# Kernel optimization log

Measured on AMD Instinct MI355X. Metric: run time of the kernel, lower is better.

Reference implementation:

```python
import jax, jax.numpy as jnp
import numpy as np

NUM_SAMPLES = 10
MIN_DIST_PTS = 8
TOP_K = 10
GRID_SIZE = 4
GAP = 0.1


def sample_line_points(seg):
    # seg: [N,2,2] (endpoints, ij coords). Vectorized version of the per-group linspace loop.
    lengths = jnp.linalg.norm(seg[:, 0] - seg[:, 1], axis=1)
    n_samp = jnp.clip(jnp.floor(lengths / MIN_DIST_PTS), 2, NUM_SAMPLES)  # [N]
    t = jnp.arange(NUM_SAMPLES, dtype=seg.dtype)  # [S]
    interval = (seg[:, 1] - seg[:, 0]) / (n_samp[:, None] - 1)  # [N,2]
    pts = seg[:, None, 0, :] + t[None, :, None] * interval[:, None, :]  # [N,S,2]
    valid = t[None, :] < n_samp[:, None]  # [N,S]
    pts = jnp.where(valid[..., None], pts, 0.0)  # original zero-pads invalid samples
    return pts, valid


def grid_sample_norm(desc, pts, img_size):
    # desc: [D,Hc,Wc]; pts: [P,2] (i,j) pixel coords in image of size img_size=(H,W).
    # Replicates kornia normalize_pixel_coordinates + F.grid_sample(align_corners=False,
    # bilinear, zero padding), then L2-normalize along D.
    D, Hc, Wc = desc.shape
    H, W = img_size
    gx = 2.0 * pts[:, 1] / (W - 1) - 1.0
    gy = 2.0 * pts[:, 0] / (H - 1) - 1.0
    ix = ((gx + 1.0) * Wc - 1.0) / 2.0
    iy = ((gy + 1.0) * Hc - 1.0) / 2.0
    x0 = jnp.floor(ix)
    y0 = jnp.floor(iy)
    wx1 = ix - x0
    wy1 = iy - y0
    x0i = x0.astype(jnp.int32)
    y0i = y0.astype(jnp.int32)

    def gather(yi, xi):
        inb = (xi >= 0) & (xi < Wc) & (yi >= 0) & (yi < Hc)
        v = desc[:, jnp.clip(yi, 0, Hc - 1), jnp.clip(xi, 0, Wc - 1)]  # [D,P]
        return v * inb

    v = (gather(y0i, x0i) * (1 - wy1) * (1 - wx1)
         + gather(y0i, x0i + 1) * (1 - wy1) * wx1
         + gather(y0i + 1, x0i) * wy1 * (1 - wx1)
         + gather(y0i + 1, x0i + 1) * wy1 * wx1)
    nrm = jnp.linalg.norm(v, axis=0, keepdims=True)
    return v / jnp.maximum(nrm, 1e-12)


def needleman_wunsch(scores):
    # scores: [B,n,m]. Row-wise scan; the within-row dependency
    # v[j+1]=max(v[j], max(prev[j+1], prev[j]+s)) is a prefix-max (cummax).
    b, n, m = scores.shape
    s = scores - GAP
    init = jnp.zeros((b, m + 1), s.dtype)

    def step(prev, row):  # prev [B,m+1], row [B,m]
        a = jnp.maximum(prev[:, 1:], prev[:, :-1] + row)
        new = jnp.maximum(jax.lax.cummax(a, axis=1), 0.0)
        return jnp.concatenate([jnp.zeros((b, 1), s.dtype), new], axis=1), None

    final, _ = jax.lax.scan(step, init, jnp.swapaxes(s, 0, 1))
    return final[:, -1]


def nw_candidate_scores(scores):
    # scores: [N1,N2,S,S] -> (nw [N1,2k], topk [N1,k])
    ls1 = jnp.max(scores, axis=3)
    v1 = ls1 != -1
    ls1 = jnp.where(v1, ls1, 0.0).sum(2) / v1.sum(2)
    ls2 = jnp.max(scores, axis=2)
    v2 = ls2 != -1
    ls2 = jnp.where(v2, ls2, 0.0).sum(2) / v2.sum(2)
    line_scores = (ls1 + ls2) / 2
    topk = jnp.argsort(line_scores, axis=1)[:, -TOP_K:]  # [N1,k]
    top_scores = jnp.take_along_axis(scores, topk[:, :, None, None], axis=1)  # [N1,k,S,S]
    top_scores = jnp.concatenate([top_scores, jnp.flip(top_scores, axis=-1)], axis=1)  # [N1,2k,S,S]
    N1, t2k, n, m = top_scores.shape
    nw = needleman_wunsch(top_scores.reshape(N1 * t2k, n, m)).reshape(N1, t2k)
    return nw, topk


def filter_and_match(scores):
    nw, topk = nw_candidate_scores(scores)
    t2k = nw.shape[1]
    best = jnp.argmax(nw, axis=1) % (t2k // 2)
    return jnp.take_along_axis(topk, best[:, None], axis=1)[:, 0]


def compute_scores(line_seg1, line_seg2, desc1, desc2):
    S = NUM_SAMPLES
    img1 = (desc1.shape[2] * GRID_SIZE, desc1.shape[3] * GRID_SIZE)
    img2 = (desc2.shape[2] * GRID_SIZE, desc2.shape[3] * GRID_SIZE)
    pts1, val1 = sample_line_points(line_seg1)
    pts2, val2 = sample_line_points(line_seg2)
    d1 = grid_sample_norm(desc1[0], pts1.reshape(-1, 2), img1)  # [D, N1*S]
    d2 = grid_sample_norm(desc2[0], pts2.reshape(-1, 2), img2)  # [D, N2*S]
    sc = d1.T @ d2  # [N1*S, N2*S]
    sc = jnp.where(val1.reshape(-1)[:, None], sc, -1.0)
    sc = jnp.where(val2.reshape(-1)[None, :], sc, -1.0)
    N1, N2 = line_seg1.shape[0], line_seg2.shape[0]
    return sc.reshape(N1, S, N2, S).transpose(0, 2, 1, 3)  # [N1,N2,S,S]


def reference(line_seg1, line_seg2, desc1, desc2):
    scores = compute_scores(line_seg1, line_seg2, desc1, desc2)
    matches = filter_and_match(scores)
    # cross check
    matches2 = filter_and_match(scores.transpose(1, 0, 3, 2))
    mutual = matches2[matches] == jnp.arange(line_seg1.shape[0])
    return jnp.where(mutual, matches, -1).astype(jnp.int32)


def setup_inputs() -> dict:
    key = jax.random.key(0)
    k1, k2, k3, k4 = jax.random.split(key, 4)
    IMG = 512.0
    line_seg1 = jax.random.uniform(k1, (512, 2, 2), dtype=jnp.float32) * (IMG - 1.0)
    line_seg2 = jax.random.uniform(k2, (512, 2, 2), dtype=jnp.float32) * (IMG - 1.0)
    desc1 = jax.random.normal(k3, (1, 128, 128, 128), dtype=jnp.float32)
    desc2 = jax.random.normal(k4, (1, 128, 128, 128), dtype=jnp.float32)
    return {"line_seg1": line_seg1, "line_seg2": line_seg2, "desc1": desc1, "desc2": desc2}
```

## Files before the change

### kernel.cpp

```cpp
#include <hip/hip_runtime.h>
#include <cmath>

#define NL 512
#define SS 10
#define DD 128
#define HWC (128 * 128)

typedef _Float16 f16x8 __attribute__((ext_vector_type(8)));
typedef float f32x4 __attribute__((ext_vector_type(4)));

__device__ __forceinline__ void gload_lds16(const void* g, void* l)
{
    __builtin_amdgcn_global_load_lds(
        (__attribute__((address_space(1))) void*)const_cast<void*>(g),
        (__attribute__((address_space(3))) void*)l, 16, 0, 0);
}

__global__ __launch_bounds__(256) void transpose_kernel(
    const float* __restrict__ in1, const float* __restrict__ in2,
    float* __restrict__ out1, float* __restrict__ out2)
{
    const float* in = blockIdx.z ? in2 : in1;
    float* out = blockIdx.z ? out2 : out1;
    __shared__ float tile[32][33];
    int hw0 = blockIdx.x * 32;
    int d0 = blockIdx.y * 32;
    int tx = threadIdx.x, ty = threadIdx.y;
#pragma unroll
    for (int j = 0; j < 32; j += 8)
        tile[ty + j][tx] = in[(size_t)(d0 + ty + j) * HWC + hw0 + tx];
    __syncthreads();
#pragma unroll
    for (int j = 0; j < 32; j += 8)
        out[(size_t)(hw0 + ty + j) * DD + d0 + tx] = tile[tx][ty + j];
}

__device__ __forceinline__ float fetchd(const float* __restrict__ dt, int y, int x, int d)
{
    bool inb = (x >= 0) && (x < 128) && (y >= 0) && (y < 128);
    int yc = y < 0 ? 0 : (y > 127 ? 127 : y);
    int xc = x < 0 ? 0 : (x > 127 ? 127 : x);
    float v = dt[((size_t)(yc * 128 + xc)) * DD + d];
    return inb ? v : 0.0f;
}

__global__ __launch_bounds__(256) void sample_kernel(
    const float* __restrict__ seg1, const float* __restrict__ seg2,
    const float* __restrict__ dt1, const float* __restrict__ dt2,
    float* __restrict__ dd1, float* __restrict__ dd2,
    _Float16* __restrict__ h1, _Float16* __restrict__ m1,
    _Float16* __restrict__ h2, _Float16* __restrict__ m2,
    int* __restrict__ v1, int* __restrict__ v2)
{
#pragma clang fp contract(off)
    int L = blockIdx.x;
    int img = blockIdx.y;
    const float* seg = img ? seg2 : seg1;
    const float* dt = img ? dt2 : dt1;
    float* dd = img ? dd2 : dd1;
    _Float16* ph = img ? h2 : h1;
    _Float16* pm = img ? m2 : m1;
    int* vv = img ? v2 : v1;

    float p0y = seg[L * 4 + 0], p0x = seg[L * 4 + 1];
    float p1y = seg[L * 4 + 2], p1x = seg[L * 4 + 3];
    float dy = p0y - p1y, dx = p0x - p1x;
    float len = sqrtf(dy * dy + dx * dx);
    float nf = floorf(len / 8.0f);
    nf = fminf(fmaxf(nf, 2.0f), 10.0f);
    int ni = (int)nf;
    float ivy = (p1y - p0y) / (nf - 1.0f);
    float ivx = (p1x - p0x) / (nf - 1.0f);

    int tid = threadIdx.x;
    int g = tid >> 7;
    int d = tid & 127;
    __shared__ float redw[4];

    for (int it = 0; it < 5; ++it) {
        int t = it * 2 + g;
        int pt = L * SS + t;
        bool val = t < ni;
        float v = 0.0f, s = 0.0f;
        if (val) {
            float py = p0y + (float)t * ivy;
            float px = p0x + (float)t * ivx;
            float gx = 2.0f * px / 511.0f - 1.0f;
            float gy = 2.0f * py / 511.0f - 1.0f;
            float ix = ((gx + 1.0f) * 128.0f - 1.0f) / 2.0f;
            float iy = ((gy + 1.0f) * 128.0f - 1.0f) / 2.0f;
            float x0f = floorf(ix), y0f = floorf(iy);
            float wx = ix - x0f, wy = iy - y0f;
            int x0 = (int)x0f, y0 = (int)y0f;
            float g00 = fetchd(dt, y0, x0, d);
            float g01 = fetchd(dt, y0, x0 + 1, d);
            float g10 = fetchd(dt, y0 + 1, x0, d);
            float g11 = fetchd(dt, y0 + 1, x0 + 1, d);
            float omwx = 1.0f - wx, omwy = 1.0f - wy;
            v = g00 * omwy * omwx + g01 * omwy * wx + g10 * wy * omwx + g11 * wy * wx;
            s = v * v;
        }
#pragma unroll
        for (int m = 1; m < 64; m <<= 1) s += __shfl_xor(s, m);
        if ((tid & 63) == 0) redw[tid >> 6] = s;
        __syncthreads();
        float outv = 0.0f;
        if (val) {
            float nrm = sqrtf(redw[2 * g] + redw[2 * g + 1]);
            outv = v / fmaxf(nrm, 1e-12f);
        }
        dd[(size_t)pt * DD + d] = outv;
        float xs = outv * 256.0f;
        _Float16 hh = (_Float16)xs;
        float r1 = xs - (float)hh;
        _Float16 mm = (_Float16)r1;
        int po = ((pt >> 4) << 11) + ((d >> 3) << 7) + ((pt & 15) << 3) + (d & 7);
        ph[po] = hh;
        pm[po] = mm;
        if (d == 0) vv[pt] = val ? 1 : 0;
        __syncthreads();
    }
}

__device__ __forceinline__ void stage_ks(
    const _Float16* __restrict__ ah, const _Float16* __restrict__ am,
    const _Float16* __restrict__ bh, const _Float16* __restrict__ bm,
    int bi, int bj, int ks, int wave, int lane, char* dst)
{
#pragma unroll
    for (int c = 0; c < 10; ++c) {
        int chunk = wave * 10 + c;
        int side = chunk >= 20;
        int rem = side ? chunk - 20 : chunk;
        int plane = rem >= 10;
        int pb = plane ? rem - 10 : rem;
        const _Float16* base = side ? (plane ? bm : bh) : (plane ? am : ah);
        size_t off = ((size_t)((side ? bj : bi) * 10 + pb) << 11) + (ks << 9) + (lane << 3);
        gload_lds16(base + off, dst + (chunk << 10));
    }
}

__global__ __launch_bounds__(256, 2) void gemm_ls_kernel(
    const _Float16* __restrict__ ah_, const _Float16* __restrict__ am_,
    const _Float16* __restrict__ bh_, const _Float16* __restrict__ bm_,
    const int* __restrict__ v1, const int* __restrict__ v2,
    float* __restrict__ ls, float* __restrict__ lsT)
{
    __shared__ __align__(16) char smem[81920];
    int tid = threadIdx.x;
    int wave = tid >> 6, lane = tid & 63;
    int wr = wave >> 1, wc = wave & 1;

    int flat = blockIdx.y * 32 + blockIdx.x;
    int xcd = flat & 7, n = flat >> 3;
    int bi = (xcd >> 1) * 8 + (n >> 4);
    int bj = (xcd & 1) * 16 + (n & 15);

    int fro = ((lane >> 4) << 8) + ((lane & 15) << 4);

    f32x4 zz = {0.0f, 0.0f, 0.0f, 0.0f};
    f32x4 acc[5][5];
#pragma unroll
    for (int i = 0; i < 5; ++i)
#pragma unroll
        for (int j = 0; j < 5; ++j) acc[i][j] = zz;

    stage_ks(ah_, am_, bh_, bm_, bi, bj, 0, wave, lane, smem);

#pragma unroll 1
    for (int ks = 0; ks < 4; ++ks) {
        char* buf = smem + ((ks & 1) ? 40960 : 0);
        if (ks < 3) {
            stage_ks(ah_, am_, bh_, bm_, bi, bj, ks + 1, wave, lane,
                     smem + (((ks + 1) & 1) ? 40960 : 0));
            asm volatile("s_waitcnt vmcnt(10)" ::: "memory");
        } else {
            asm volatile("s_waitcnt vmcnt(0)" ::: "memory");
        }
        __builtin_amdgcn_sched_barrier(0);
        __builtin_amdgcn_s_barrier();
        __builtin_amdgcn_sched_barrier(0);

        f16x8 B0[5], B1[5];
#pragma unroll
        for (int j = 0; j < 5; ++j) {
            int pb = wc * 5 + j;
            B0[j] = *(const f16x8*)(buf + ((20 + pb) << 10) + fro);
            B1[j] = *(const f16x8*)(buf + ((30 + pb) << 10) + fro);
        }
#pragma unroll
        for (int i = 0; i < 5; ++i) {
            int pb = wr * 5 + i;
            f16x8 fh = *(const f16x8*)(buf + (pb << 10) + fro);
            f16x8 fm = *(const f16x8*)(buf + ((10 + pb) << 10) + fro);
#pragma unroll
            for (int j = 0; j < 5; ++j) {
                f32x4 t = acc[i][j];
                t = __builtin_amdgcn_mfma_f32_16x16x32_f16(fh, B0[j], t, 0, 0, 0);
                t = __builtin_amdgcn_mfma_f32_16x16x32_f16(fh, B1[j], t, 0, 0, 0);
                t = __builtin_amdgcn_mfma_f32_16x16x32_f16(fm, B0[j], t, 0, 0, 0);
                acc[i][j] = t;
            }
        }
        __builtin_amdgcn_sched_barrier(0);
        __builtin_amdgcn_s_barrier();
        __builtin_amdgcn_sched_barrier(0);
    }

    float* scr = (float*)smem;
    const float rescale = 1.0f / 65536.0f;
    for (int half = 0; half < 2; ++half) {
        __syncthreads();
        if (wr == half) {
            float* reg = scr + wc * 6464;
#pragma unroll
            for (int i = 0; i < 5; ++i)
#pragma unroll
                for (int j = 0; j < 5; ++j)
#pragma unroll
                    for (int r = 0; r < 4; ++r) {
                        int row = i * 16 + ((lane >> 4) << 2) + r;
                        int col = j * 16 + (lane & 15);
                        int pi = row / 10, s = row - pi * 10;
                        int pj = col / 10, t = col - pj * 10;
                        reg[(pi * 8 + pj) * 101 + s * 10 + t] = acc[i][j][r] * rescale;
                    }
            asm volatile("s_waitcnt lgkmcnt(0)" ::: "memory");
            const float* mp = reg + lane * 101;
            int iL = bi * 16 + half * 8 + (lane >> 3);
            int jL = bj * 16 + wc * 8 + (lane & 7);
            int va[10], vb[10];
#pragma unroll
            for (int s = 0; s < 10; ++s) va[s] = v1[iL * 10 + s];
#pragma unroll
            for (int t = 0; t < 10; ++t) vb[t] = v2[jL * 10 + t];
            float cmx[10];
#pragma unroll
            for (int t = 0; t < 10; ++t) cmx[t] = -3.0e38f;
            float sum1 = 0.0f; int c1 = 0;
#pragma unroll
            for (int s = 0; s < 10; ++s) {
                float rmx = -3.0e38f;
#pragma unroll
                for (int t = 0; t < 10; ++t) {
                    float v = (va[s] && vb[t]) ? mp[s * 10 + t] : -1.0f;
                    rmx = fmaxf(rmx, v);
                    cmx[t] = fmaxf(cmx[t], v);
                }
                if (rmx != -1.0f) { sum1 += rmx; c1++; }
            }
            float sum2 = 0.0f; int c2 = 0;
#pragma unroll
            for (int t = 0; t < 10; ++t) {
                if (cmx[t] != -1.0f) { sum2 += cmx[t]; c2++; }
            }
            float out = (sum1 / (float)c1 + sum2 / (float)c2) * 0.5f;
            ls[(size_t)iL * NL + jL] = out;
            lsT[(size_t)jL * NL + iL] = out;
        }
    }
}

__global__ __launch_bounds__(64) void topk_kernel(
    const float* __restrict__ ls, const float* __restrict__ lsT, int* __restrict__ topk)
{
    int i = blockIdx.x;
    int dir = blockIdx.y;
    int lane = threadIdx.x;
    const float* src = dir ? &lsT[(size_t)i * NL] : &ls[(size_t)i * NL];

    float v[8];
#pragma unroll
    for (int it = 0; it < 8; ++it) v[it] = src[it * 64 + lane];
    int* outp = &topk[(size_t)(dir * NL + i) * 10];

    for (int p = 9; p >= 0; --p) {
        float bv = -3.0e38f;
        int bi = -1;
#pragma unroll
        for (int it = 0; it < 8; ++it) {
            int j = it * 64 + lane;
            bool better = (v[it] > bv) || (v[it] == bv && j > bi);
            if (better) { bv = v[it]; bi = j; }
        }
#pragma unroll
        for (int m = 1; m < 64; m <<= 1) {
            float ov = __shfl_xor(bv, m);
            int oi = __shfl_xor(bi, m);
            bool better = (ov > bv) || (ov == bv && oi > bi);
            if (better) { bv = ov; bi = oi; }
        }
        if ((bi & 63) == lane) v[bi >> 6] = -3.0e38f;
        if (lane == 0) outp[p] = bi;
    }
}

__global__ __launch_bounds__(128) void nw_kernel(
    const float* __restrict__ d1, const float* __restrict__ d2,
    const int* __restrict__ v1, const int* __restrict__ v2,
    const int* __restrict__ topk, float* __restrict__ nwout)
{
    int L = blockIdx.x;
    int dir = blockIdx.y;
    const float* Ad = dir ? d2 : d1;
    const float* Bd = dir ? d1 : d2;
    const int* vA = dir ? v2 : v1;
    const int* vB = dir ? v1 : v2;
    const int* tk = topk + (size_t)(dir * NL + L) * 10;

    __shared__ float Asl[10 * 132];
    __shared__ float Bsl[10 * 132];
    __shared__ float M[10][110];
    __shared__ int vam[10];

    int tid = threadIdx.x;
#pragma unroll
    for (int it = 0; it < 10; ++it) {
        int idx = tid + it * 128;
        int row = idx >> 7, col = idx & 127;
        Asl[row * 132 + col] = Ad[((size_t)L * 10 + row) * DD + col];
    }
    if (tid < 10) vam[tid] = vA[L * 10 + tid];

    for (int c = 0; c < 10; ++c) {
        int j = tk[c];
        __syncthreads();
#pragma unroll
        for (int it = 0; it < 10; ++it) {
            int idx = tid + it * 128;
            int row = idx >> 7, col = idx & 127;
            Bsl[row * 132 + col] = Bd[((size_t)j * 10 + row) * DD + col];
        }
        __syncthreads();
        if (tid < 100) {
            int s = tid / 10, t = tid - s * 10;
            const float4* ap = (const float4*)&Asl[s * 132];
            const float4* bp = (const float4*)&Bsl[t * 132];
            float acc = 0.0f;
#pragma unroll
            for (int k = 0; k < 32; ++k) {
                float4 a = ap[k], b = bp[k];
                acc = fmaf(a.x, b.x, acc);
                acc = fmaf(a.y, b.y, acc);
                acc = fmaf(a.z, b.z, acc);
                acc = fmaf(a.w, b.w, acc);
            }
            int ok = vam[s] && vB[j * 10 + t];
            M[c][s * 11 + t] = ok ? acc : -1.0f;
        }
    }
    __syncthreads();

    if (tid < 20) {
        int c = tid % 10, f = tid / 10;
        float prev[11];
#pragma unroll
        for (int p = 0; p < 11; ++p) prev[p] = 0.0f;
#pragma unroll
        for (int s = 0; s < 10; ++s) {
            float oldp = prev[0];
            float run = -3.0e38f;
#pragma unroll
            for (int t = 0; t < 10; ++t) {
                int tt = f ? (9 - t) : t;
                float sc = M[c][s * 11 + tt] - 0.1f;
                float pt1 = prev[t + 1];
                float av = fmaxf(pt1, oldp + sc);
                run = fmaxf(run, av);
                prev[t + 1] = fmaxf(run, 0.0f);
                oldp = pt1;
            }
        }
        nwout[((size_t)(dir * NL + L)) * 20 + f * 10 + c] = prev[10];
    }
}

__global__ __launch_bounds__(512) void final_kernel(
    const float* __restrict__ nw, const int* __restrict__ topk, int* __restrict__ out)
{
    __shared__ int m1[NL], m2[NL];
    int t = threadIdx.x;
    {
        const float* p = nw + (size_t)t * 20;
        float bb = -3.0e38f; int kk = 0;
        for (int k = 0; k < 20; ++k) {
            float v = p[k];
            if (v > bb) { bb = v; kk = k; }
        }
        m1[t] = topk[(size_t)t * 10 + (kk % 10)];
    }
    {
        const float* p = nw + (size_t)(NL + t) * 20;
        float bb = -3.0e38f; int kk = 0;
        for (int k = 0; k < 20; ++k) {
            float v = p[k];
            if (v > bb) { bb = v; kk = k; }
        }
        m2[t] = topk[(size_t)(NL + t) * 10 + (kk % 10)];
    }
    __syncthreads();
    int mt = m1[t];
    out[t] = (m2[mt] == t) ? mt : -1;
}

extern "C" void kernel_launch(void* const* d_in, const int* in_sizes, int n_in,
                              void* d_out, int out_size, void* d_ws, size_t ws_size,
                              hipStream_t stream)
{
    const float* seg1 = (const float*)d_in[0];
    const float* seg2 = (const float*)d_in[1];
    const float* desc1 = (const float*)d_in[2];
    const float* desc2 = (const float*)d_in[3];
    int* out = (int*)d_out;

    char* ws = (char*)d_ws;
    size_t off = 0;
    float* dt1 = (float*)(ws + off); off += (size_t)DD * HWC * 4;
    float* dt2 = (float*)(ws + off); off += (size_t)DD * HWC * 4;
    float* dd1 = (float*)(ws + off); off += (size_t)NL * SS * DD * 4;
    float* dd2 = (float*)(ws + off); off += (size_t)NL * SS * DD * 4;
    int* v1 = (int*)(ws + off); off += (size_t)NL * SS * 4;
    int* v2 = (int*)(ws + off); off += (size_t)NL * SS * 4;
    float* ls = (float*)(ws + off); off += (size_t)NL * NL * 4;
    float* lsT = (float*)(ws + off); off += (size_t)NL * NL * 4;
    int* topk = (int*)(ws + off); off += (size_t)2 * NL * 10 * 4;
    float* nwv = (float*)(ws + off); off += (size_t)2 * NL * 20 * 4;
    size_t PL = (size_t)NL * SS * DD;
    _Float16* h1 = (_Float16*)(ws + off); off += PL * 2;
    _Float16* m1 = (_Float16*)(ws + off); off += PL * 2;
    _Float16* h2 = (_Float16*)(ws + off); off += PL * 2;
    _Float16* m2 = (_Float16*)(ws + off); off += PL * 2;

    transpose_kernel<<<dim3(HWC / 32, DD / 32, 2), dim3(32, 8), 0, stream>>>(
        desc1, desc2, dt1, dt2);
    sample_kernel<<<dim3(NL, 2), 256, 0, stream>>>(
        seg1, seg2, dt1, dt2, dd1, dd2, h1, m1, h2, m2, v1, v2);
    gemm_ls_kernel<<<dim3(32, 32), 256, 0, stream>>>(
        h1, m1, h2, m2, v1, v2, ls, lsT);
    topk_kernel<<<dim3(NL, 2), 64, 0, stream>>>(ls, lsT, topk);
    nw_kernel<<<dim3(NL, 2), 128, 0, stream>>>(dd1, dd2, v1, v2, topk, nwv);
    final_kernel<<<1, 512, 0, stream>>>(nwv, topk, out);
}
```

Baseline: 183.8 us.

## Restructure sample and NW kernels for wider parallelism and fewer barriers

The sample kernel now uses one wave per sample point (640 threads, each lane handling two channels), so the norm reduction is a pure wave shuffle with no shared memory or block barriers and no serial loop over samples. The NW kernel now loads all ten top-k candidate descriptor blocks into shared memory at once and computes all 1000 dot products in parallel with 256 threads, instead of ten serial load/sync/compute rounds. The cost is larger shared memory per NW block (about 53KB), which limits how many blocks fit per CU, and larger sample blocks.

```diff
diff --git a/kernel.cpp b/kernel.cpp
--- a/kernel.cpp
+++ b/kernel.cpp
@@ -44,7 +44,7 @@
     return inb ? v : 0.0f;
 }
 
-__global__ __launch_bounds__(256) void sample_kernel(
+__global__ __launch_bounds__(640) void sample_kernel(
     const float* __restrict__ seg1, const float* __restrict__ seg2,
     const float* __restrict__ dt1, const float* __restrict__ dt2,
     float* __restrict__ dd1, float* __restrict__ dd2,
@@ -72,54 +72,51 @@
     float ivy = (p1y - p0y) / (nf - 1.0f);
     float ivx = (p1x - p0x) / (nf - 1.0f);
 
-    int tid = threadIdx.x;
-    int g = tid >> 7;
-    int d = tid & 127;
-    __shared__ float redw[4];
-
-    for (int it = 0; it < 5; ++it) {
-        int t = it * 2 + g;
-        int pt = L * SS + t;
-        bool val = t < ni;
-        float v = 0.0f, s = 0.0f;
-        if (val) {
-            float py = p0y + (float)t * ivy;
-            float px = p0x + (float)t * ivx;
-            float gx = 2.0f * px / 511.0f - 1.0f;
-            float gy = 2.0f * py / 511.0f - 1.0f;
-            float ix = ((gx + 1.0f) * 128.0f - 1.0f) / 2.0f;
-            float iy = ((gy + 1.0f) * 128.0f - 1.0f) / 2.0f;
-            float x0f = floorf(ix), y0f = floorf(iy);
-            float wx = ix - x0f, wy = iy - y0f;
-            int x0 = (int)x0f, y0 = (int)y0f;
-            float g00 = fetchd(dt, y0, x0, d);
-            float g01 = fetchd(dt, y0, x0 + 1, d);
-            float g10 = fetchd(dt, y0 + 1, x0, d);
-            float g11 = fetchd(dt, y0 + 1, x0 + 1, d);
-            float omwx = 1.0f - wx, omwy = 1.0f - wy;
-            v = g00 * omwy * omwx + g01 * omwy * wx + g10 * wy * omwx + g11 * wy * wx;
-            s = v * v;
-        }
+    int t = threadIdx.x >> 6;
+    int lane = threadIdx.x & 63;
+    int pt = L * SS + t;
+    bool val = t < ni;
+    int d0 = lane, d1 = lane + 64;
+    float o0 = 0.0f, o1 = 0.0f;
+    if (val) {
+        float py = p0y + (float)t * ivy;
+        float px = p0x + (float)t * ivx;
+        float gx = 2.0f * px / 511.0f - 1.0f;
+        float gy = 2.0f * py / 511.0f - 1.0f;
+        float ix = ((gx + 1.0f) * 128.0f - 1.0f) / 2.0f;
+        float iy = ((gy + 1.0f) * 128.0f - 1.0f) / 2.0f;
+        float x0f = floorf(ix), y0f = floorf(iy);
+        float wx = ix - x0f, wy = iy - y0f;
+        int x0 = (int)x0f, y0 = (int)y0f;
+        float a00 = fetchd(dt, y0, x0, d0),         b00 = fetchd(dt, y0, x0, d1);
+        float a01 = fetchd(dt, y0, x0 + 1, d0),     b01 = fetchd(dt, y0, x0 + 1, d1);
+        float a10 = fetchd(dt, y0 + 1, x0, d0),     b10 = fetchd(dt, y0 + 1, x0, d1);
+        float a11 = fetchd(dt, y0 + 1, x0 + 1, d0), b11 = fetchd(dt, y0 + 1, x0 + 1, d1);
+        float omwx = 1.0f - wx, omwy = 1.0f - wy;
+        float va = a00 * omwy * omwx + a01 * omwy * wx + a10 * wy * omwx + a11 * wy * wx;
+        float vb = b00 * omwy * omwx + b01 * omwy * wx + b10 * wy * omwx + b11 * wy * wx;
+        float s = va * va + vb * vb;
 #pragma unroll
         for (int m = 1; m < 64; m <<= 1) s += __shfl_xor(s, m);
-        if ((tid & 63) == 0) redw[tid >> 6] = s;
-        __syncthreads();
-        float outv = 0.0f;
-        if (val) {
-            float nrm = sqrtf(redw[2 * g] + redw[2 * g + 1]);
-            outv = v / fmaxf(nrm, 1e-12f);
-        }
-        dd[(size_t)pt * DD + d] = outv;
-        float xs = outv * 256.0f;
-        _Float16 hh = (_Float16)xs;
-        float r1 = xs - (float)hh;
-        _Float16 mm = (_Float16)r1;
-        int po = ((pt >> 4) << 11) + ((d >> 3) << 7) + ((pt & 15) << 3) + (d & 7);
-        ph[po] = hh;
-        pm[po] = mm;
-        if (d == 0) vv[pt] = val ? 1 : 0;
-        __syncthreads();
-    }
+        float nrm = sqrtf(s);
+        float inv = 1.0f;
+        o0 = va / fmaxf(nrm, 1e-12f);
+        o1 = vb / fmaxf(nrm, 1e-12f);
+        (void)inv;
+    }
+    dd[(size_t)pt * DD + d0] = o0;
+    dd[(size_t)pt * DD + d1] = o1;
+    float xs0 = o0 * 256.0f;
+    _Float16 hh0 = (_Float16)xs0;
+    _Float16 mm0 = (_Float16)(xs0 - (float)hh0);
+    float xs1 = o1 * 256.0f;
+    _Float16 hh1 = (_Float16)xs1;
+    _Float16 mm1 = (_Float16)(xs1 - (float)hh1);
+    int po0 = ((pt >> 4) << 11) + ((d0 >> 3) << 7) + ((pt & 15) << 3) + (d0 & 7);
+    int po1 = ((pt >> 4) << 11) + ((d1 >> 3) << 7) + ((pt & 15) << 3) + (d1 & 7);
+    ph[po0] = hh0; pm[po0] = mm0;
+    ph[po1] = hh1; pm[po1] = mm1;
+    if (lane == 0) vv[pt] = val ? 1 : 0;
 }
 
 __device__ __forceinline__ void stage_ks(
@@ -295,7 +292,7 @@
     }
 }
 
-__global__ __launch_bounds__(128) void nw_kernel(
+__global__ __launch_bounds__(256) void nw_kernel(
     const float* __restrict__ d1, const float* __restrict__ d2,
     const int* __restrict__ v1, const int* __restrict__ v2,
     const int* __restrict__ topk, float* __restrict__ nwout)
@@ -309,33 +306,37 @@
     const int* tk = topk + (size_t)(dir * NL + L) * 10;
 
     __shared__ float Asl[10 * 132];
-    __shared__ float Bsl[10 * 132];
+    __shared__ float Bsl[10][1320];
     __shared__ float M[10][110];
-    __shared__ int vam[10];
+    __shared__ int vam[10], tks[10];
 
     int tid = threadIdx.x;
-#pragma unroll
-    for (int it = 0; it < 10; ++it) {
-        int idx = tid + it * 128;
+    if (tid < 10) { vam[tid] = vA[L * 10 + tid]; tks[tid] = tk[tid]; }
+#pragma unroll
+    for (int it = 0; it < 5; ++it) {
+        int idx = tid + it * 256;
         int row = idx >> 7, col = idx & 127;
         Asl[row * 132 + col] = Ad[((size_t)L * 10 + row) * DD + col];
     }
-    if (tid < 10) vam[tid] = vA[L * 10 + tid];
-
-    for (int c = 0; c < 10; ++c) {
-        int j = tk[c];
-        __syncthreads();
-#pragma unroll
-        for (int it = 0; it < 10; ++it) {
-            int idx = tid + it * 128;
-            int row = idx >> 7, col = idx & 127;
-            Bsl[row * 132 + col] = Bd[((size_t)j * 10 + row) * DD + col];
-        }
-        __syncthreads();
-        if (tid < 100) {
-            int s = tid / 10, t = tid - s * 10;
+    __syncthreads();
+#pragma unroll
+    for (int it = 0; it < 50; ++it) {
+        int idx = tid + it * 256;
+        int c = idx / 1280;
+        int rem = idx - c * 1280;
+        int row = rem >> 7, col = rem & 127;
+        Bsl[c][row * 132 + col] = Bd[((size_t)tks[c] * 10 + row) * DD + col];
+    }
+    __syncthreads();
+#pragma unroll
+    for (int it = 0; it < 4; ++it) {
+        int w = tid + it * 256;
+        if (w < 1000) {
+            int c = w / 100;
+            int rem = w - c * 100;
+            int s = rem / 10, t = rem - s * 10;
             const float4* ap = (const float4*)&Asl[s * 132];
-            const float4* bp = (const float4*)&Bsl[t * 132];
+            const float4* bp = (const float4*)&Bsl[c][t * 132];
             float acc = 0.0f;
 #pragma unroll
             for (int k = 0; k < 32; ++k) {
@@ -345,7 +346,7 @@
                 acc = fmaf(a.z, b.z, acc);
                 acc = fmaf(a.w, b.w, acc);
             }
-            int ok = vam[s] && vB[j * 10 + t];
+            int ok = vam[s] && vB[tks[c] * 10 + t];
             M[c][s * 11 + t] = ok ? acc : -1.0f;
         }
     }
@@ -433,11 +434,11 @@
 
     transpose_kernel<<<dim3(HWC / 32, DD / 32, 2), dim3(32, 8), 0, stream>>>(
         desc1, desc2, dt1, dt2);
-    sample_kernel<<<dim3(NL, 2), 256, 0, stream>>>(
+    sample_kernel<<<dim3(NL, 2), 640, 0, stream>>>(
         seg1, seg2, dt1, dt2, dd1, dd2, h1, m1, h2, m2, v1, v2);
     gemm_ls_kernel<<<dim3(32, 32), 256, 0, stream>>>(
         h1, m1, h2, m2, v1, v2, ls, lsT);
     topk_kernel<<<dim3(NL, 2), 64, 0, stream>>>(ls, lsT, topk);
-    nw_kernel<<<dim3(NL, 2), 128, 0, stream>>>(dd1, dd2, v1, v2, topk, nwv);
+    nw_kernel<<<dim3(NL, 2), 256, 0, stream>>>(dd1, dd2, v1, v2, topk, nwv);
     final_kernel<<<1, 512, 0, stream>>>(nwv, topk, out);
 }
```

New measurement: 183.7 us. About the same (-0.1%).
